# Performance work log

Hardware: AMD Instinct MI355X
Metric: run time of the kernel (lower is better)

Reference implementation:

```python
import jax, jax.numpy as jnp
import numpy as np


def setup_inputs() -> dict:
    key = jax.random.key(0)
    k1, k2 = jax.random.split(key)
    x = jax.random.normal(k1, (16384, 4096), dtype=jnp.float32)
    # parameter initialized uniform(-0.01, 0.01) in the original
    v = jax.random.uniform(k2, (4096, 256), dtype=jnp.float32, minval=-0.01, maxval=0.01)
    return {"x": x, "v": v}


def reference(x, v):
    # FM second-order term: sum_{i<j} (v_i . v_j) x_i x_j
    # = 0.5 * (||x @ v||^2 - sum_f (x^2 @ v^2)_f), per batch row.
    xv = jnp.einsum('bn,nf->bf', x, v)            # [B, F]
    x2v2 = jnp.einsum('bn,nf->bf', x * x, v * v)  # [B, F]
    res = 0.5 * jnp.sum(xv * xv - x2v2, axis=-1, keepdims=True)  # [B, 1]
    return res
```

## Files before the change

### kernel.cpp

```cpp
#include <hip/hip_runtime.h>
#include <hip/hip_bf16.h>

#define B_DIM 16384
#define K_DIM 4096
#define F_DIM 256
#define BM 64
#define BK 64
#define NSTEP (K_DIM / BK)

typedef short bf16x8 __attribute__((ext_vector_type(8)));
typedef float f32x4 __attribute__((ext_vector_type(4)));

static __device__ __forceinline__ ushort f2bf(float f) {
    union { __hip_bfloat16 h; ushort s; } u;
    u.h = __float2bfloat16(f);
    return u.s;
}

static __device__ __forceinline__ void gload_lds16(const void* g, void* l) {
    __builtin_amdgcn_global_load_lds(
        (const __attribute__((address_space(1))) unsigned int*)g,
        (__attribute__((address_space(3))) unsigned int*)l, 16, 0, 0);
}

__global__ __launch_bounds__(512) void prep_w(const float* __restrict__ v,
                                              float* __restrict__ w) {
    const int lane = threadIdx.x & 63;
    const int n = blockIdx.x * 8 + (threadIdx.x >> 6);
    const float4 vv = *reinterpret_cast<const float4*>(v + (size_t)n * F_DIM + lane * 4);
    float s = vv.x * vv.x + vv.y * vv.y + vv.z * vv.z + vv.w * vv.w;
#pragma unroll
    for (int m = 1; m < 64; m <<= 1) s += __shfl_xor(s, m);
    if (lane == 0) w[n] = s;
}

__global__ __launch_bounds__(512) void prep_t(const float* __restrict__ v,
                                              ushort* __restrict__ vT) {
    __shared__ ushort T[256][72];
    const int tid = threadIdx.x;
    const int n0 = blockIdx.x * 64;
    const int wid = tid >> 6;
    const int f0 = (tid & 63) * 4;
#pragma unroll
    for (int j = 0; j < 8; ++j) {
        const int r = j * 8 + wid;
        const float4 vv = *reinterpret_cast<const float4*>(v + (size_t)(n0 + r) * F_DIM + f0);
        T[f0 + 0][r] = f2bf(vv.x);
        T[f0 + 1][r] = f2bf(vv.y);
        T[f0 + 2][r] = f2bf(vv.z);
        T[f0 + 3][r] = f2bf(vv.w);
    }
    __syncthreads();
    const int nb = (tid & 7) * 8;
#pragma unroll
    for (int s = 0; s < 4; ++s) {
        const int f = s * 64 + (tid >> 3);
        const uint4 val = *reinterpret_cast<const uint4*>(&T[f][nb]);
        *reinterpret_cast<uint4*>(vT + (size_t)f * K_DIM + n0 + nb) = val;
    }
}

__global__ __launch_bounds__(512) void fm_kernel(const float* __restrict__ x,
                                                 const ushort* __restrict__ vT,
                                                 const float* __restrict__ w,
                                                 float* __restrict__ out) {
    __shared__ ushort Ab[2][BM * BK];
    __shared__ ushort Bb[2][F_DIM * BK];
    __shared__ float red[BM][4];
    __shared__ float s2red[BM];

    const int tid = threadIdx.x;
    const int lane = tid & 63;
    const int wid = tid >> 6;
    const int wr = wid >> 2;
    const int wc = wid & 3;
    const int mbase = blockIdx.x * BM;

    const int sr = tid >> 4;
    const int sc = (tid & 15) * 4;
    const float* gx1 = x + (size_t)(mbase + sr) * K_DIM + sc;
    const float* gx2 = x + (size_t)(mbase + 32 + sr) * K_DIM + sc;
    const float* gw = w + sc;
    const int aW1 = sr * 128 + ((sc * 2) ^ ((sr & 7) << 4));
    const int aW2 = (32 + sr) * 128 + ((sc * 2) ^ ((sr & 7) << 4));
    int bsrc[4];
#pragma unroll
    for (int i = 0; i < 4; ++i) {
        const int o = i * 8192 + tid * 16;
        const int col = o >> 7;
        const int j = o & 127;
        bsrc[i] = col * 8192 + (j ^ ((col & 7) << 4));
    }
    const char* vTb = reinterpret_cast<const char*>(vT);

    int aRo[2], aXm[2], bRo[4], bXm[4];
#pragma unroll
    for (int m = 0; m < 2; ++m) {
        const int r = wr * 32 + m * 16 + (lane & 15);
        aRo[m] = r * 128;
        aXm[m] = (r & 7) << 4;
    }
#pragma unroll
    for (int n = 0; n < 4; ++n) {
        const int c = wc * 64 + n * 16 + (lane & 15);
        bRo[n] = c * 128;
        bXm[n] = (c & 7) << 4;
    }
    const int kl = (lane >> 4) * 16;

    float s2a = 0.f, s2b = 0.f;
    f32x4 acc[2][4] = {};
    float4 va, vb, wv;

    auto stage_load = [&](int k0, int buf) {
        va = *reinterpret_cast<const float4*>(gx1 + k0);
        vb = *reinterpret_cast<const float4*>(gx2 + k0);
        wv = *reinterpret_cast<const float4*>(gw + k0);
        char* bdst = reinterpret_cast<char*>(&Bb[buf][0]) + wid * 1024;
        const char* bs = vTb + (size_t)k0 * 2;
#pragma unroll
        for (int i = 0; i < 4; ++i)
            gload_lds16(bs + bsrc[i], bdst + i * 8192);
    };
    auto stage_store = [&](int buf) {
        s2a += va.x * va.x * wv.x + va.y * va.y * wv.y
             + va.z * va.z * wv.z + va.w * va.w * wv.w;
        s2b += vb.x * vb.x * wv.x + vb.y * vb.y * wv.y
             + vb.z * vb.z * wv.z + vb.w * vb.w * wv.w;
        uint2 pa, pb;
        pa.x = (uint)f2bf(va.x) | ((uint)f2bf(va.y) << 16);
        pa.y = (uint)f2bf(va.z) | ((uint)f2bf(va.w) << 16);
        pb.x = (uint)f2bf(vb.x) | ((uint)f2bf(vb.y) << 16);
        pb.y = (uint)f2bf(vb.z) | ((uint)f2bf(vb.w) << 16);
        char* abase = reinterpret_cast<char*>(&Ab[buf][0]);
        *reinterpret_cast<uint2*>(abase + aW1) = pa;
        *reinterpret_cast<uint2*>(abase + aW2) = pb;
    };

    stage_load(0, 0);
    stage_store(0);
    __syncthreads();

    for (int kt = 0; kt < NSTEP; ++kt) {
        const int cur = kt & 1;
        const bool pf = (kt + 1) < NSTEP;
        if (pf) stage_load((kt + 1) * BK, cur ^ 1);

        const char* Ac = reinterpret_cast<const char*>(&Ab[cur][0]);
        const char* Bc = reinterpret_cast<const char*>(&Bb[cur][0]);
        bf16x8 af[2][2], bfr[4][2];
#pragma unroll
        for (int m = 0; m < 2; ++m)
#pragma unroll
            for (int ks = 0; ks < 2; ++ks)
                af[m][ks] = *reinterpret_cast<const bf16x8*>(
                    Ac + aRo[m] + ((kl + ks * 64) ^ aXm[m]));
#pragma unroll
        for (int n = 0; n < 4; ++n)
#pragma unroll
            for (int ks = 0; ks < 2; ++ks)
                bfr[n][ks] = *reinterpret_cast<const bf16x8*>(
                    Bc + bRo[n] + ((kl + ks * 64) ^ bXm[n]));
#pragma unroll
        for (int ks = 0; ks < 2; ++ks)
#pragma unroll
            for (int m = 0; m < 2; ++m)
#pragma unroll
                for (int n = 0; n < 4; ++n)
                    acc[m][n] = __builtin_amdgcn_mfma_f32_16x16x32_bf16(
                        af[m][ks], bfr[n][ks], acc[m][n], 0, 0, 0);

        if (pf) stage_store(cur ^ 1);
        __syncthreads();
    }

#pragma unroll
    for (int m = 0; m < 2; ++m) {
#pragma unroll
        for (int j = 0; j < 4; ++j) {
            float s = 0.f;
#pragma unroll
            for (int n = 0; n < 4; ++n) {
                const float y = acc[m][n][j];
                s += y * y;
            }
            s += __shfl_xor(s, 1);
            s += __shfl_xor(s, 2);
            s += __shfl_xor(s, 4);
            s += __shfl_xor(s, 8);
            if ((lane & 15) == 0)
                red[wr * 32 + m * 16 + (lane >> 4) * 4 + j][wc] = s;
        }
    }
    s2a += __shfl_xor(s2a, 1); s2a += __shfl_xor(s2a, 2);
    s2a += __shfl_xor(s2a, 4); s2a += __shfl_xor(s2a, 8);
    s2b += __shfl_xor(s2b, 1); s2b += __shfl_xor(s2b, 2);
    s2b += __shfl_xor(s2b, 4); s2b += __shfl_xor(s2b, 8);
    if ((tid & 15) == 0) {
        s2red[sr] = s2a;
        s2red[32 + sr] = s2b;
    }
    __syncthreads();
    if (tid < BM) {
        const float s1 = red[tid][0] + red[tid][1] + red[tid][2] + red[tid][3];
        out[mbase + tid] = 0.5f * (s1 - s2red[tid]);
    }
}

extern "C" void kernel_launch(void* const* d_in, const int* in_sizes, int n_in,
                              void* d_out, int out_size, void* d_ws, size_t ws_size,
                              hipStream_t stream) {
    const float* x = (const float*)d_in[0];
    const float* v = (const float*)d_in[1];
    float* out = (float*)d_out;

    ushort* vT = (ushort*)d_ws;
    float* w = (float*)((char*)d_ws + (size_t)F_DIM * K_DIM * sizeof(ushort));

    prep_w<<<K_DIM / 8, 512, 0, stream>>>(v, w);
    prep_t<<<K_DIM / 64, 512, 0, stream>>>(v, vT);
    fm_kernel<<<B_DIM / BM, 512, 0, stream>>>(x, vT, w, out);
}
```

Measured before the change: 417.8 us.

## Stream fp32 x into LDS directly and read vT fragments from global into registers

The FM kernel is restructured to 32-row blocks of 256 threads. x tiles are copied as fp32 straight into LDS with global_load_lds and converted to bf16 at fragment-read time, and the vT operand is no longer staged through LDS; each wave loads its B fragments from global (L2) into double-buffered registers. The intent is to drop the register round-trip and LDS traffic for B and raise occupancy, allowing three blocks per CU. The cost is that vT is re-read from L2 by every block, twice as many blocks now do so, and the sum-of-squares work falls on a single wave.

After: 472.4 us. +13.1%, slower.

```diff
diff --git a/kernel.cpp b/kernel.cpp
--- a/kernel.cpp
+++ b/kernel.cpp
@@ -4,7 +4,7 @@
 #define B_DIM 16384
 #define K_DIM 4096
 #define F_DIM 256
-#define BM 64
+#define BM 32
 #define BK 64
 #define NSTEP (K_DIM / BK)
 
@@ -60,107 +60,90 @@
     }
 }
 
-__global__ __launch_bounds__(512) void fm_kernel(const float* __restrict__ x,
-                                                 const ushort* __restrict__ vT,
-                                                 const float* __restrict__ w,
-                                                 float* __restrict__ out) {
-    __shared__ ushort Ab[2][BM * BK];
-    __shared__ ushort Bb[2][F_DIM * BK];
+__global__ __launch_bounds__(256, 3) void fm_kernel(const float* __restrict__ x,
+                                                    const ushort* __restrict__ vT,
+                                                    const float* __restrict__ w,
+                                                    float* __restrict__ out) {
+    __shared__ float Ab[2][BM * BK];
     __shared__ float red[BM][4];
     __shared__ float s2red[BM];
 
     const int tid = threadIdx.x;
     const int lane = tid & 63;
-    const int wid = tid >> 6;
-    const int wr = wid >> 2;
-    const int wc = wid & 3;
+    const int wc = tid >> 6;
+    const int l15 = lane & 15;
+    const int koff = lane >> 4;
+
     const int mbase = blockIdx.x * BM;
 
-    const int sr = tid >> 4;
-    const int sc = (tid & 15) * 4;
-    const float* gx1 = x + (size_t)(mbase + sr) * K_DIM + sc;
-    const float* gx2 = x + (size_t)(mbase + 32 + sr) * K_DIM + sc;
-    const float* gw = w + sc;
-    const int aW1 = sr * 128 + ((sc * 2) ^ ((sr & 7) << 4));
-    const int aW2 = (32 + sr) * 128 + ((sc * 2) ^ ((sr & 7) << 4));
-    int bsrc[4];
-#pragma unroll
-    for (int i = 0; i < 4; ++i) {
-        const int o = i * 8192 + tid * 16;
-        const int col = o >> 7;
-        const int j = o & 127;
-        bsrc[i] = col * 8192 + (j ^ ((col & 7) << 4));
-    }
-    const char* vTb = reinterpret_cast<const char*>(vT);
-
-    int aRo[2], aXm[2], bRo[4], bXm[4];
+    const int srow = tid >> 4;
+    const int sj = (tid & 15) * 16;
+    const int sjj = sj ^ ((srow & 7) << 4);
+    const float* gx1 = x + (size_t)(mbase + srow) * K_DIM + (sjj >> 2);
+    const float* gx2 = x + (size_t)(mbase + 16 + srow) * K_DIM + (sjj >> 2);
+
+    auto stageA = [&](int k0, int buf) {
+        char* base = reinterpret_cast<char*>(&Ab[buf][0]) + wc * 1024;
+        gload_lds16(gx1 + k0, base);
+        gload_lds16(gx2 + k0, base + 4096);
+    };
+
+    int aRo[2], aXm[2];
 #pragma unroll
     for (int m = 0; m < 2; ++m) {
-        const int r = wr * 32 + m * 16 + (lane & 15);
-        aRo[m] = r * 128;
+        const int r = m * 16 + l15;
+        aRo[m] = r * 256;
         aXm[m] = (r & 7) << 4;
     }
-#pragma unroll
-    for (int n = 0; n < 4; ++n) {
-        const int c = wc * 64 + n * 16 + (lane & 15);
-        bRo[n] = c * 128;
-        bXm[n] = (c & 7) << 4;
-    }
-    const int kl = (lane >> 4) * 16;
-
-    float s2a = 0.f, s2b = 0.f;
+    const int cbase = koff * 32;
+
+    const ushort* vb = vT + (size_t)(wc * 64 + l15) * K_DIM + koff * 8;
+    const float* wb = w + koff * 8;
+
     f32x4 acc[2][4] = {};
-    float4 va, vb, wv;
-
-    auto stage_load = [&](int k0, int buf) {
-        va = *reinterpret_cast<const float4*>(gx1 + k0);
-        vb = *reinterpret_cast<const float4*>(gx2 + k0);
-        wv = *reinterpret_cast<const float4*>(gw + k0);
-        char* bdst = reinterpret_cast<char*>(&Bb[buf][0]) + wid * 1024;
-        const char* bs = vTb + (size_t)k0 * 2;
-#pragma unroll
-        for (int i = 0; i < 4; ++i)
-            gload_lds16(bs + bsrc[i], bdst + i * 8192);
+    float s2m0 = 0.f, s2m1 = 0.f;
+    bf16x8 bA[4][2], bB[4][2];
+
+    auto loadB = [&](int k0, bf16x8 (&bn)[4][2]) {
+#pragma unroll
+        for (int n = 0; n < 4; ++n)
+#pragma unroll
+            for (int ks = 0; ks < 2; ++ks)
+                bn[n][ks] = *reinterpret_cast<const bf16x8*>(
+                    vb + (size_t)n * 16 * K_DIM + k0 + ks * 32);
     };
-    auto stage_store = [&](int buf) {
-        s2a += va.x * va.x * wv.x + va.y * va.y * wv.y
-             + va.z * va.z * wv.z + va.w * va.w * wv.w;
-        s2b += vb.x * vb.x * wv.x + vb.y * vb.y * wv.y
-             + vb.z * vb.z * wv.z + vb.w * vb.w * wv.w;
-        uint2 pa, pb;
-        pa.x = (uint)f2bf(va.x) | ((uint)f2bf(va.y) << 16);
-        pa.y = (uint)f2bf(va.z) | ((uint)f2bf(va.w) << 16);
-        pb.x = (uint)f2bf(vb.x) | ((uint)f2bf(vb.y) << 16);
-        pb.y = (uint)f2bf(vb.z) | ((uint)f2bf(vb.w) << 16);
-        char* abase = reinterpret_cast<char*>(&Ab[buf][0]);
-        *reinterpret_cast<uint2*>(abase + aW1) = pa;
-        *reinterpret_cast<uint2*>(abase + aW2) = pb;
-    };
-
-    stage_load(0, 0);
-    stage_store(0);
-    __syncthreads();
-
-    for (int kt = 0; kt < NSTEP; ++kt) {
-        const int cur = kt & 1;
-        const bool pf = (kt + 1) < NSTEP;
-        if (pf) stage_load((kt + 1) * BK, cur ^ 1);
-
-        const char* Ac = reinterpret_cast<const char*>(&Ab[cur][0]);
-        const char* Bc = reinterpret_cast<const char*>(&Bb[cur][0]);
-        bf16x8 af[2][2], bfr[4][2];
-#pragma unroll
-        for (int m = 0; m < 2; ++m)
-#pragma unroll
-            for (int ks = 0; ks < 2; ++ks)
-                af[m][ks] = *reinterpret_cast<const bf16x8*>(
-                    Ac + aRo[m] + ((kl + ks * 64) ^ aXm[m]));
-#pragma unroll
-        for (int n = 0; n < 4; ++n)
-#pragma unroll
-            for (int ks = 0; ks < 2; ++ks)
-                bfr[n][ks] = *reinterpret_cast<const bf16x8*>(
-                    Bc + bRo[n] + ((kl + ks * 64) ^ bXm[n]));
+
+    auto compute = [&](int k0, int buf, bf16x8 (&bc)[4][2]) {
+        const char* Ac = reinterpret_cast<const char*>(&Ab[buf][0]);
+        bf16x8 af[2][2];
+#pragma unroll
+        for (int ks = 0; ks < 2; ++ks) {
+            float4 wlo = {0, 0, 0, 0}, whi = {0, 0, 0, 0};
+            if (wc == 0) {
+                wlo = *reinterpret_cast<const float4*>(wb + k0 + ks * 32);
+                whi = *reinterpret_cast<const float4*>(wb + k0 + ks * 32 + 4);
+            }
+#pragma unroll
+            for (int m = 0; m < 2; ++m) {
+                const int c0 = (ks * 128 + cbase) ^ aXm[m];
+                const int c1 = (ks * 128 + cbase + 16) ^ aXm[m];
+                const f32x4 lo = *reinterpret_cast<const f32x4*>(Ac + aRo[m] + c0);
+                const f32x4 hi = *reinterpret_cast<const f32x4*>(Ac + aRo[m] + c1);
+                bf16x8 a;
+                a[0] = (short)f2bf(lo[0]); a[1] = (short)f2bf(lo[1]);
+                a[2] = (short)f2bf(lo[2]); a[3] = (short)f2bf(lo[3]);
+                a[4] = (short)f2bf(hi[0]); a[5] = (short)f2bf(hi[1]);
+                a[6] = (short)f2bf(hi[2]); a[7] = (short)f2bf(hi[3]);
+                af[m][ks] = a;
+                if (wc == 0) {
+                    const float t = lo[0] * lo[0] * wlo.x + lo[1] * lo[1] * wlo.y
+                                  + lo[2] * lo[2] * wlo.z + lo[3] * lo[3] * wlo.w
+                                  + hi[0] * hi[0] * whi.x + hi[1] * hi[1] * whi.y
+                                  + hi[2] * hi[2] * whi.z + hi[3] * hi[3] * whi.w;
+                    if (m == 0) s2m0 += t; else s2m1 += t;
+                }
+            }
+        }
 #pragma unroll
         for (int ks = 0; ks < 2; ++ks)
 #pragma unroll
@@ -168,9 +151,23 @@
 #pragma unroll
                 for (int n = 0; n < 4; ++n)
                     acc[m][n] = __builtin_amdgcn_mfma_f32_16x16x32_bf16(
-                        af[m][ks], bfr[n][ks], acc[m][n], 0, 0, 0);
-
-        if (pf) stage_store(cur ^ 1);
+                        af[m][ks], bc[n][ks], acc[m][n], 0, 0, 0);
+    };
+
+    stageA(0, 0);
+    loadB(0, bA);
+    __syncthreads();
+
+    for (int t = 0; t < NSTEP; t += 2) {
+        stageA((t + 1) * BK, 1);
+        loadB((t + 1) * BK, bB);
+        compute(t * BK, 0, bA);
+        __syncthreads();
+        if (t + 2 < NSTEP) {
+            stageA((t + 2) * BK, 0);
+            loadB((t + 2) * BK, bA);
+        }
+        compute((t + 1) * BK, 1, bB);
         __syncthreads();
     }
 
@@ -180,30 +177,23 @@
         for (int j = 0; j < 4; ++j) {
             float s = 0.f;
 #pragma unroll
-            for (int n = 0; n < 4; ++n) {
-                const float y = acc[m][n][j];
-                s += y * y;
-            }
+            for (int n = 0; n < 4; ++n) { const float y = acc[m][n][j]; s += y * y; }
             s += __shfl_xor(s, 1);
             s += __shfl_xor(s, 2);
             s += __shfl_xor(s, 4);
             s += __shfl_xor(s, 8);
-            if ((lane & 15) == 0)
-                red[wr * 32 + m * 16 + (lane >> 4) * 4 + j][wc] = s;
+            if (l15 == 0) red[m * 16 + koff * 4 + j][wc] = s;
         }
     }
-    s2a += __shfl_xor(s2a, 1); s2a += __shfl_xor(s2a, 2);
-    s2a += __shfl_xor(s2a, 4); s2a += __shfl_xor(s2a, 8);
-    s2b += __shfl_xor(s2b, 1); s2b += __shfl_xor(s2b, 2);
-    s2b += __shfl_xor(s2b, 4); s2b += __shfl_xor(s2b, 8);
-    if ((tid & 15) == 0) {
-        s2red[sr] = s2a;
-        s2red[32 + sr] = s2b;
+    if (wc == 0) {
+        s2m0 += __shfl_xor(s2m0, 16); s2m0 += __shfl_xor(s2m0, 32);
+        s2m1 += __shfl_xor(s2m1, 16); s2m1 += __shfl_xor(s2m1, 32);
+        if (lane < 16) { s2red[lane] = s2m0; s2red[16 + lane] = s2m1; }
     }
     __syncthreads();
     if (tid < BM) {
-        const float s1 = red[tid][0] + red[tid][1] + red[tid][2] + red[tid][3];
-        out[mbase + tid] = 0.5f * (s1 - s2red[tid]);
+        out[mbase + tid] = 0.5f * (red[tid][0] + red[tid][1] + red[tid][2]
+                                   + red[tid][3] - s2red[tid]);
     }
 }
 
@@ -219,5 +209,5 @@
 
     prep_w<<<K_DIM / 8, 512, 0, stream>>>(v, w);
     prep_t<<<K_DIM / 64, 512, 0, stream>>>(v, vT);
-    fm_kernel<<<B_DIM / BM, 512, 0, stream>>>(x, vT, w, out);
-}
+    fm_kernel<<<B_DIM / BM, 256, 0, stream>>>(x, vT, w, out);
+}
```
